# Kernel optimization log

Hardware: AMD Instinct MI355X
Metric: run time of the kernel (lower is better)

Reference implementation:

```python
import jax, jax.numpy as jnp
import numpy as np

MAX_NEIGHBORS = 10
D = 1024
N = 16384

def setup_inputs() -> dict:
    key = jax.random.key(0)
    ks = jax.random.split(key, 12)
    s = 0.05
    inp = {
        'target_embedding': jax.random.normal(ks[0], (D,), jnp.float32),
        'all_embeddings': jax.random.normal(ks[1], (N, D), jnp.float32),
        'similarity_matrix': jax.random.normal(ks[2], (N, N), jnp.float32),
        # attention_net: Linear(2D->D), ReLU, Linear(D->1)
        'W_att1': jax.random.normal(ks[3], (2 * D, D), jnp.float32) * s,
        'b_att1': jnp.zeros((D,), jnp.float32),
        'W_att2': jax.random.normal(ks[4], (D, 1), jnp.float32) * s,
        'b_att2': jnp.zeros((1,), jnp.float32),
        # neighbor_count_net: Linear(D->D//2), ReLU, Linear(D//2->1), Sigmoid
        'W_cnt1': jax.random.normal(ks[5], (D, D // 2), jnp.float32) * s,
        'b_cnt1': jnp.zeros((D // 2,), jnp.float32),
        'W_cnt2': jax.random.normal(ks[6], (D // 2, 1), jnp.float32) * s,
        'b_cnt2': jnp.zeros((1,), jnp.float32),
        'target_idx': 123,
    }
    return inp

def reference(target_embedding, all_embeddings, similarity_matrix,
              W_att1, b_att1, W_att2, b_att2,
              W_cnt1, b_cnt1, W_cnt2, b_cnt2, target_idx):
    # dynamic neighbor count: int(sigmoid(mlp(x)) * max_neighbors), clamped to [1, max_neighbors]
    h = jax.nn.relu(target_embedding @ W_cnt1 + b_cnt1)
    frac = jax.nn.sigmoid(h @ W_cnt2 + b_cnt2)[0]
    dynamic_k = jnp.clip(jnp.floor(frac * MAX_NEIGHBORS).astype(jnp.int32), 1, MAX_NEIGHBORS)

    # top-(K+1) over the target's similarity row; statically sized, mask to dynamic_k
    row = similarity_matrix[target_idx]
    _, top_idx = jax.lax.top_k(row, MAX_NEIGHBORS + 1)  # [K+1]
    # stable compaction: move target_idx (if present) to the end, keep order otherwise
    order = jnp.where(top_idx == target_idx, MAX_NEIGHBORS + 1, jnp.arange(MAX_NEIGHBORS + 1))
    neighbor_idx = top_idx[jnp.argsort(order)][:MAX_NEIGHBORS]  # [K]
    valid = jnp.arange(MAX_NEIGHBORS) < dynamic_k              # [K]

    neighbor_emb = all_embeddings[neighbor_idx]                 # [K, D]
    target_exp = jnp.broadcast_to(target_embedding, (MAX_NEIGHBORS, D))
    pair = jnp.concatenate([target_exp, neighbor_emb], axis=-1)  # [K, 2D]
    scores = (jax.nn.relu(pair @ W_att1 + b_att1) @ W_att2 + b_att2)[:, 0]  # [K]
    scores = jnp.where(valid, scores, -jnp.inf)
    weights = jax.nn.softmax(scores)                            # zeros at invalid slots
    aggregated = weights @ neighbor_emb                         # [D]
    return aggregated, weights, neighbor_idx, weights
```

## Files before the change

kernel.cpp:

```cpp
#include <hip/hip_runtime.h>
#include <math.h>

#define NN 16384
#define DD 1024
#define HD 512

#define WS_DK  0
#define WS_NB  4
#define WS_UV  32
#define WS_HP  11296

__global__ void k_phaseA(const float* __restrict__ x, const float* __restrict__ Wc1,
                         const float* __restrict__ sim, const int* __restrict__ tidx,
                         float* __restrict__ ws, float* __restrict__ out) {
    const int t = threadIdx.x;
    const int b = blockIdx.x;
    if (b != 0) {
        __shared__ float xs[32];
        const int c = b - 1;
        const int ibase = c * 32;
        if (t < 32) xs[t] = x[ibase + t];
        __syncthreads();
        float acc = 0.f;
        const float* W = Wc1 + (size_t)ibase * HD + t;
        #pragma unroll 8
        for (int ii = 0; ii < 32; ++ii) acc += xs[ii] * W[(size_t)ii * HD];
        ws[WS_HP + c * HD + t] = acc;
        return;
    }

    for (int i = t; i < 11 * DD; i += 512) ws[WS_UV + i] = 0.f;

    const int tgt = tidx[0];
    const float4* row4 = (const float4*)(sim + (size_t)tgt * NN);
    float vals[32];
    #pragma unroll
    for (int c = 0; c < 8; ++c) {
        float4 v = row4[c * 512 + t];
        vals[c * 4 + 0] = v.x; vals[c * 4 + 1] = v.y;
        vals[c * 4 + 2] = v.z; vals[c * 4 + 3] = v.w;
    }
    unsigned used = 0u;

    __shared__ float wvs[8];
    __shared__ int   wgs[8];
    __shared__ int   winner;
    __shared__ int   toplist[11];
    const int lane = t & 63, wave = t >> 6;

    for (int it = 0; it < 11; ++it) {
        float bv = -INFINITY; int bs = 0;
        #pragma unroll
        for (int s = 0; s < 32; ++s) {
            float v = ((used >> s) & 1u) ? -INFINITY : vals[s];
            if (v > bv) { bv = v; bs = s; }
        }
        int gi = (bs >> 2) * 2048 + t * 4 + (bs & 3);
        for (int off = 32; off > 0; off >>= 1) {
            float ov = __shfl_down(bv, off);
            int   og = __shfl_down(gi, off);
            if (ov > bv || (ov == bv && og < gi)) { bv = ov; gi = og; }
        }
        if (lane == 0) { wvs[wave] = bv; wgs[wave] = gi; }
        __syncthreads();
        if (t == 0) {
            float fv = wvs[0]; int fg = wgs[0];
            for (int w = 1; w < 8; ++w)
                if (wvs[w] > fv || (wvs[w] == fv && wgs[w] < fg)) { fv = wvs[w]; fg = wgs[w]; }
            toplist[it] = fg;
            winner = fg;
        }
        __syncthreads();
        int w = winner;
        if (((w >> 2) & 511) == t) used |= 1u << ((w >> 11) * 4 + (w & 3));
    }
    if (t == 0) {
        int cnt = 0;
        int* nb = (int*)ws + WS_NB;
        for (int i = 0; i < 11 && cnt < 10; ++i) {
            int v = toplist[i];
            if (v != tgt) { nb[cnt] = v; out[1034 + cnt] = (float)v; ++cnt; }
        }
    }
}

__global__ void k_phaseB(const float* __restrict__ x, const float* __restrict__ emb,
                         const float* __restrict__ W1, const float* __restrict__ bc1,
                         const float* __restrict__ Wc2, const float* __restrict__ bc2,
                         float* __restrict__ ws) {
    const int t = threadIdx.x;
    const int b = blockIdx.x;
    if (b == 128) {
        __shared__ float red[256];
        float acc = 0.f;
        #pragma unroll
        for (int jj = 0; jj < 2; ++jj) {
            int j = t + jj * 256;
            float s = 0.f;
            #pragma unroll 8
            for (int c = 0; c < 32; ++c) s += ws[WS_HP + c * HD + j];
            float h = fmaxf(s + bc1[j], 0.f);
            acc += h * Wc2[j];
        }
        red[t] = acc;
        __syncthreads();
        for (int off = 128; off > 0; off >>= 1) {
            if (t < off) red[t] += red[t + off];
            __syncthreads();
        }
        if (t == 0) {
            float z = red[0] + bc2[0];
            float frac = 1.f / (1.f + expf(-z));
            int dk = (int)floorf(frac * 10.f);
            ((int*)ws)[WS_DK] = dk < 1 ? 1 : (dk > 10 ? 10 : dk);
        }
        return;
    }
    __shared__ float xs[32];
    __shared__ float es[10][32];
    __shared__ int   nb[10];
    const int jc = b & 3;
    const int ic = b >> 2;
    const int ibase = ic * 32;
    const int j = jc * 256 + t;
    if (t < 10) nb[t] = ((const int*)ws)[WS_NB + t];
    if (t < 32) xs[t] = x[ibase + t];
    __syncthreads();
    for (int idx = t; idx < 320; idx += 256) {
        int k = idx >> 5, ii = idx & 31;
        es[k][ii] = emb[(size_t)nb[k] * DD + ibase + ii];
    }
    __syncthreads();
    float acc[11];
    #pragma unroll
    for (int k = 0; k < 11; ++k) acc[k] = 0.f;
    const float* Wt = W1 + (size_t)ibase * DD + j;
    const float* Wb = W1 + (size_t)(1024 + ibase) * DD + j;
    for (int ii = 0; ii < 32; ++ii) {
        float wt = Wt[(size_t)ii * DD];
        float wb = Wb[(size_t)ii * DD];
        acc[10] += xs[ii] * wt;
        #pragma unroll
        for (int k = 0; k < 10; ++k) acc[k] += es[k][ii] * wb;
    }
    #pragma unroll
    for (int k = 0; k < 11; ++k) atomicAdd(&ws[WS_UV + k * DD + j], acc[k]);
}

__global__ void k_phaseC(const float* __restrict__ emb, const float* __restrict__ ba1,
                         const float* __restrict__ W2, const float* __restrict__ ba2,
                         float* __restrict__ ws, float* __restrict__ out) {
    const int t = threadIdx.x;
    const int wave = t >> 6, lane = t & 63;
    __shared__ float sc[10];
    __shared__ float wl[10];
    __shared__ int   nbs[10];
    if (t < 10) nbs[t] = ((const int*)ws)[WS_NB + t];
    if (wave < 10) {
        float acc = 0.f;
        #pragma unroll
        for (int m = 0; m < 16; ++m) {
            int j = lane + m * 64;
            float h = ws[WS_UV + 10 * DD + j] + ws[WS_UV + wave * DD + j] + ba1[j];
            acc += fmaxf(h, 0.f) * W2[j];
        }
        #pragma unroll
        for (int off = 32; off > 0; off >>= 1) acc += __shfl_down(acc, off);
        if (lane == 0) sc[wave] = acc + ba2[0];
    }
    __syncthreads();
    if (t == 0) {
        int dk = ((const int*)ws)[WS_DK];
        float v[10];
        float m = -INFINITY;
        for (int k = 0; k < 10; ++k) {
            v[k] = (k < dk) ? sc[k] : -INFINITY;
            if (v[k] > m) m = v[k];
        }
        float sum = 0.f;
        for (int k = 0; k < 10; ++k) { v[k] = expf(v[k] - m); sum += v[k]; }
        for (int k = 0; k < 10; ++k) wl[k] = v[k] / sum;
    }
    __syncthreads();
    float a = 0.f;
    #pragma unroll
    for (int k = 0; k < 10; ++k) a += wl[k] * emb[(size_t)nbs[k] * DD + t];
    out[t] = a;
    if (t < 10) { out[1024 + t] = wl[t]; out[1044 + t] = wl[t]; }
}

extern "C" void kernel_launch(void* const* d_in, const int* in_sizes, int n_in,
                              void* d_out, int out_size, void* d_ws, size_t ws_size,
                              hipStream_t stream) {
    const float* x    = (const float*)d_in[0];
    const float* emb  = (const float*)d_in[1];
    const float* sim  = (const float*)d_in[2];
    const float* W1   = (const float*)d_in[3];
    const float* ba1  = (const float*)d_in[4];
    const float* W2   = (const float*)d_in[5];
    const float* ba2  = (const float*)d_in[6];
    const float* Wc1  = (const float*)d_in[7];
    const float* bc1  = (const float*)d_in[8];
    const float* Wc2  = (const float*)d_in[9];
    const float* bc2  = (const float*)d_in[10];
    const int*   tidx = (const int*)d_in[11];
    float* out = (float*)d_out;
    float* ws  = (float*)d_ws;

    hipLaunchKernelGGL(k_phaseA, dim3(33),  dim3(512),  0, stream, x, Wc1, sim, tidx, ws, out);
    hipLaunchKernelGGL(k_phaseB, dim3(129), dim3(256),  0, stream, x, emb, W1, bc1, Wc2, bc2, ws);
    hipLaunchKernelGGL(k_phaseC, dim3(1),   dim3(1024), 0, stream, emb, ba1, W2, ba2, ws, out);
}
```

Before: 38.36 us.

## Fuse three phases into one cooperative kernel with grid syncs and W1 prefetch

Replaces the three separate kernel launches with one cooperative kernel of 129 blocks that uses grid-wide syncs between the phases. While the top-k block runs, idle blocks pre-read their W1 slices to warm the cache for the attention matvec. The goal is to remove launch gaps between kernels and hide the W1 load latency behind the serial top-k. In exchange it adds grid.sync overhead and cooperative-launch constraints, and the top-k now runs on 256 threads with 64 values per thread instead of 512 threads.

```diff
diff --git a/kernel.cpp b/kernel.cpp
--- a/kernel.cpp
+++ b/kernel.cpp
@@ -1,5 +1,8 @@
 #include <hip/hip_runtime.h>
+#include <hip/hip_cooperative_groups.h>
 #include <math.h>
+
+namespace cg = cooperative_groups;
 
 #define NN 16384
 #define DD 1024
@@ -10,88 +13,129 @@
 #define WS_UV  32
 #define WS_HP  11296
 
-__global__ void k_phaseA(const float* __restrict__ x, const float* __restrict__ Wc1,
-                         const float* __restrict__ sim, const int* __restrict__ tidx,
-                         float* __restrict__ ws, float* __restrict__ out) {
+__global__ void k_fused(const float* __restrict__ x, const float* __restrict__ emb,
+                        const float* __restrict__ sim, const float* __restrict__ W1,
+                        const float* __restrict__ ba1, const float* __restrict__ W2,
+                        const float* __restrict__ ba2, const float* __restrict__ Wc1,
+                        const float* __restrict__ bc1, const float* __restrict__ Wc2,
+                        const float* __restrict__ bc2, const int* __restrict__ tidx,
+                        float* __restrict__ ws, float* __restrict__ out) {
+    cg::grid_group grid = cg::this_grid();
     const int t = threadIdx.x;
     const int b = blockIdx.x;
-    if (b != 0) {
-        __shared__ float xs[32];
-        const int c = b - 1;
-        const int ibase = c * 32;
-        if (t < 32) xs[t] = x[ibase + t];
-        __syncthreads();
-        float acc = 0.f;
-        const float* W = Wc1 + (size_t)ibase * HD + t;
-        #pragma unroll 8
-        for (int ii = 0; ii < 32; ++ii) acc += xs[ii] * W[(size_t)ii * HD];
-        ws[WS_HP + c * HD + t] = acc;
-        return;
-    }
-
-    for (int i = t; i < 11 * DD; i += 512) ws[WS_UV + i] = 0.f;
-
-    const int tgt = tidx[0];
-    const float4* row4 = (const float4*)(sim + (size_t)tgt * NN);
-    float vals[32];
-    #pragma unroll
-    for (int c = 0; c < 8; ++c) {
-        float4 v = row4[c * 512 + t];
-        vals[c * 4 + 0] = v.x; vals[c * 4 + 1] = v.y;
-        vals[c * 4 + 2] = v.z; vals[c * 4 + 3] = v.w;
-    }
-    unsigned used = 0u;
-
-    __shared__ float wvs[8];
-    __shared__ int   wgs[8];
+    const int lane = t & 63, wave = t >> 6;
+
+    __shared__ float xs[32];
+    __shared__ float es[10][32];
+    __shared__ int   nb[10];
+    __shared__ float wvs[4];
+    __shared__ int   wgs[4];
     __shared__ int   winner;
     __shared__ int   toplist[11];
-    const int lane = t & 63, wave = t >> 6;
-
-    for (int it = 0; it < 11; ++it) {
-        float bv = -INFINITY; int bs = 0;
-        #pragma unroll
-        for (int s = 0; s < 32; ++s) {
-            float v = ((used >> s) & 1u) ? -INFINITY : vals[s];
-            if (v > bv) { bv = v; bs = s; }
-        }
-        int gi = (bs >> 2) * 2048 + t * 4 + (bs & 3);
-        for (int off = 32; off > 0; off >>= 1) {
-            float ov = __shfl_down(bv, off);
-            int   og = __shfl_down(gi, off);
-            if (ov > bv || (ov == bv && og < gi)) { bv = ov; gi = og; }
-        }
-        if (lane == 0) { wvs[wave] = bv; wgs[wave] = gi; }
-        __syncthreads();
+    __shared__ float red[256];
+    __shared__ float sc[10];
+    __shared__ float wl[10];
+
+    if (b < 32) {
+        const int ibase = b * 32;
+        if (t < 32) xs[t] = x[ibase + t];
+        __syncthreads();
+        #pragma unroll
+        for (int jj = 0; jj < 2; ++jj) {
+            const int j = t + jj * 256;
+            float acc = 0.f;
+            const float* W = Wc1 + (size_t)ibase * HD + j;
+            #pragma unroll 8
+            for (int ii = 0; ii < 32; ++ii) acc += xs[ii] * W[(size_t)ii * HD];
+            ws[WS_HP + b * HD + j] = acc;
+        }
+    } else if (b == 32) {
+        for (int i = t; i < 11 * DD; i += 256) ws[WS_UV + i] = 0.f;
+    } else if (b == 33) {
+        const int tgt = tidx[0];
+        const float4* row4 = (const float4*)(sim + (size_t)tgt * NN);
+        float vals[64];
+        #pragma unroll
+        for (int c = 0; c < 16; ++c) {
+            float4 v = row4[c * 256 + t];
+            vals[c * 4 + 0] = v.x; vals[c * 4 + 1] = v.y;
+            vals[c * 4 + 2] = v.z; vals[c * 4 + 3] = v.w;
+        }
+        unsigned long long used = 0ull;
+        for (int it = 0; it < 11; ++it) {
+            float bv = -INFINITY; int bs = 0;
+            #pragma unroll
+            for (int s = 0; s < 64; ++s) {
+                float v = ((used >> s) & 1ull) ? -INFINITY : vals[s];
+                if (v > bv) { bv = v; bs = s; }
+            }
+            int gi = (bs >> 2) * 1024 + t * 4 + (bs & 3);
+            for (int off = 32; off > 0; off >>= 1) {
+                float ov = __shfl_down(bv, off);
+                int   og = __shfl_down(gi, off);
+                if (ov > bv || (ov == bv && og < gi)) { bv = ov; gi = og; }
+            }
+            if (lane == 0) { wvs[wave] = bv; wgs[wave] = gi; }
+            __syncthreads();
+            if (t == 0) {
+                float fv = wvs[0]; int fg = wgs[0];
+                for (int w = 1; w < 4; ++w)
+                    if (wvs[w] > fv || (wvs[w] == fv && wgs[w] < fg)) { fv = wvs[w]; fg = wgs[w]; }
+                toplist[it] = fg;
+                winner = fg;
+            }
+            __syncthreads();
+            int w = winner;
+            if (((w >> 2) & 255) == t) used |= 1ull << ((w >> 10) * 4 + (w & 3));
+        }
         if (t == 0) {
-            float fv = wvs[0]; int fg = wgs[0];
-            for (int w = 1; w < 8; ++w)
-                if (wvs[w] > fv || (wvs[w] == fv && wgs[w] < fg)) { fv = wvs[w]; fg = wgs[w]; }
-            toplist[it] = fg;
-            winner = fg;
-        }
-        __syncthreads();
-        int w = winner;
-        if (((w >> 2) & 511) == t) used |= 1u << ((w >> 11) * 4 + (w & 3));
+            int cnt = 0;
+            int* nbp = (int*)ws + WS_NB;
+            for (int i = 0; i < 11 && cnt < 10; ++i) {
+                int v = toplist[i];
+                if (v != tgt) { nbp[cnt] = v; out[1034 + cnt] = (float)v; ++cnt; }
+            }
+        }
+    } else if (b < 128) {
+        const int jc = b & 3, ic = b >> 2;
+        const int ibase = ic * 32;
+        const int j = jc * 256 + t;
+        float s = 0.f;
+        const float* Wt = W1 + (size_t)ibase * DD + j;
+        const float* Wb = W1 + (size_t)(1024 + ibase) * DD + j;
+        for (int ii = 0; ii < 32; ++ii) s += Wt[(size_t)ii * DD] + Wb[(size_t)ii * DD];
+        if (s == -1e30f) ws[WS_UV] = s;
     }
-    if (t == 0) {
-        int cnt = 0;
-        int* nb = (int*)ws + WS_NB;
-        for (int i = 0; i < 11 && cnt < 10; ++i) {
-            int v = toplist[i];
-            if (v != tgt) { nb[cnt] = v; out[1034 + cnt] = (float)v; ++cnt; }
-        }
-    }
-}
-
-__global__ void k_phaseB(const float* __restrict__ x, const float* __restrict__ emb,
-                         const float* __restrict__ W1, const float* __restrict__ bc1,
-                         const float* __restrict__ Wc2, const float* __restrict__ bc2,
-                         float* __restrict__ ws) {
-    const int t = threadIdx.x;
-    const int b = blockIdx.x;
-    if (b == 128) {
-        __shared__ float red[256];
+
+    grid.sync();
+
+    if (b < 128) {
+        const int jc = b & 3, ic = b >> 2;
+        const int ibase = ic * 32;
+        const int j = jc * 256 + t;
+        if (t < 10) nb[t] = ((const int*)ws)[WS_NB + t];
+        if (t < 32) xs[t] = x[ibase + t];
+        __syncthreads();
+        for (int idx = t; idx < 320; idx += 256) {
+            int k = idx >> 5, ii = idx & 31;
+            es[k][ii] = emb[(size_t)nb[k] * DD + ibase + ii];
+        }
+        __syncthreads();
+        float acc[11];
+        #pragma unroll
+        for (int k = 0; k < 11; ++k) acc[k] = 0.f;
+        const float* Wt = W1 + (size_t)ibase * DD + j;
+        const float* Wb = W1 + (size_t)(1024 + ibase) * DD + j;
+        for (int ii = 0; ii < 32; ++ii) {
+            float wt = Wt[(size_t)ii * DD];
+            float wb = Wb[(size_t)ii * DD];
+            acc[10] += xs[ii] * wt;
+            #pragma unroll
+            for (int k = 0; k < 10; ++k) acc[k] += es[k][ii] * wb;
+        }
+        #pragma unroll
+        for (int k = 0; k < 11; ++k) atomicAdd(&ws[WS_UV + k * DD + j], acc[k]);
+    } else {
         float acc = 0.f;
         #pragma unroll
         for (int jj = 0; jj < 2; ++jj) {
@@ -114,79 +158,49 @@
             int dk = (int)floorf(frac * 10.f);
             ((int*)ws)[WS_DK] = dk < 1 ? 1 : (dk > 10 ? 10 : dk);
         }
-        return;
     }
-    __shared__ float xs[32];
-    __shared__ float es[10][32];
-    __shared__ int   nb[10];
-    const int jc = b & 3;
-    const int ic = b >> 2;
-    const int ibase = ic * 32;
-    const int j = jc * 256 + t;
-    if (t < 10) nb[t] = ((const int*)ws)[WS_NB + t];
-    if (t < 32) xs[t] = x[ibase + t];
-    __syncthreads();
-    for (int idx = t; idx < 320; idx += 256) {
-        int k = idx >> 5, ii = idx & 31;
-        es[k][ii] = emb[(size_t)nb[k] * DD + ibase + ii];
+
+    grid.sync();
+
+    if (b == 0) {
+        if (t < 10) nb[t] = ((const int*)ws)[WS_NB + t];
+        __syncthreads();
+        for (int k = wave; k < 10; k += 4) {
+            float acc = 0.f;
+            #pragma unroll
+            for (int m = 0; m < 16; ++m) {
+                int j = lane + m * 64;
+                float h = ws[WS_UV + 10 * DD + j] + ws[WS_UV + k * DD + j] + ba1[j];
+                acc += fmaxf(h, 0.f) * W2[j];
+            }
+            #pragma unroll
+            for (int off = 32; off > 0; off >>= 1) acc += __shfl_down(acc, off);
+            if (lane == 0) sc[k] = acc + ba2[0];
+        }
+        __syncthreads();
+        if (t == 0) {
+            int dk = ((const int*)ws)[WS_DK];
+            float v[10];
+            float m = -INFINITY;
+            for (int k = 0; k < 10; ++k) {
+                v[k] = (k < dk) ? sc[k] : -INFINITY;
+                if (v[k] > m) m = v[k];
+            }
+            float sum = 0.f;
+            for (int k = 0; k < 10; ++k) { v[k] = expf(v[k] - m); sum += v[k]; }
+            for (int k = 0; k < 10; ++k) wl[k] = v[k] / sum;
+        }
+        __syncthreads();
+        #pragma unroll
+        for (int jj = 0; jj < 4; ++jj) {
+            int j = t + jj * 256;
+            float a = 0.f;
+            #pragma unroll
+            for (int k = 0; k < 10; ++k) a += wl[k] * emb[(size_t)nb[k] * DD + j];
+            out[j] = a;
+        }
+        if (t < 10) { out[1024 + t] = wl[t]; out[1044 + t] = wl[t]; }
     }
-    __syncthreads();
-    float acc[11];
-    #pragma unroll
-    for (int k = 0; k < 11; ++k) acc[k] = 0.f;
-    const float* Wt = W1 + (size_t)ibase * DD + j;
-    const float* Wb = W1 + (size_t)(1024 + ibase) * DD + j;
-    for (int ii = 0; ii < 32; ++ii) {
-        float wt = Wt[(size_t)ii * DD];
-        float wb = Wb[(size_t)ii * DD];
-        acc[10] += xs[ii] * wt;
-        #pragma unroll
-        for (int k = 0; k < 10; ++k) acc[k] += es[k][ii] * wb;
-    }
-    #pragma unroll
-    for (int k = 0; k < 11; ++k) atomicAdd(&ws[WS_UV + k * DD + j], acc[k]);
-}
-
-__global__ void k_phaseC(const float* __restrict__ emb, const float* __restrict__ ba1,
-                         const float* __restrict__ W2, const float* __restrict__ ba2,
-                         float* __restrict__ ws, float* __restrict__ out) {
-    const int t = threadIdx.x;
-    const int wave = t >> 6, lane = t & 63;
-    __shared__ float sc[10];
-    __shared__ float wl[10];
-    __shared__ int   nbs[10];
-    if (t < 10) nbs[t] = ((const int*)ws)[WS_NB + t];
-    if (wave < 10) {
-        float acc = 0.f;
-        #pragma unroll
-        for (int m = 0; m < 16; ++m) {
-            int j = lane + m * 64;
-            float h = ws[WS_UV + 10 * DD + j] + ws[WS_UV + wave * DD + j] + ba1[j];
-            acc += fmaxf(h, 0.f) * W2[j];
-        }
-        #pragma unroll
-        for (int off = 32; off > 0; off >>= 1) acc += __shfl_down(acc, off);
-        if (lane == 0) sc[wave] = acc + ba2[0];
-    }
-    __syncthreads();
-    if (t == 0) {
-        int dk = ((const int*)ws)[WS_DK];
-        float v[10];
-        float m = -INFINITY;
-        for (int k = 0; k < 10; ++k) {
-            v[k] = (k < dk) ? sc[k] : -INFINITY;
-            if (v[k] > m) m = v[k];
-        }
-        float sum = 0.f;
-        for (int k = 0; k < 10; ++k) { v[k] = expf(v[k] - m); sum += v[k]; }
-        for (int k = 0; k < 10; ++k) wl[k] = v[k] / sum;
-    }
-    __syncthreads();
-    float a = 0.f;
-    #pragma unroll
-    for (int k = 0; k < 10; ++k) a += wl[k] * emb[(size_t)nbs[k] * DD + t];
-    out[t] = a;
-    if (t < 10) { out[1024 + t] = wl[t]; out[1044 + t] = wl[t]; }
 }
 
 extern "C" void kernel_launch(void* const* d_in, const int* in_sizes, int n_in,
@@ -207,7 +221,8 @@
     float* out = (float*)d_out;
     float* ws  = (float*)d_ws;
 
-    hipLaunchKernelGGL(k_phaseA, dim3(33),  dim3(512),  0, stream, x, Wc1, sim, tidx, ws, out);
-    hipLaunchKernelGGL(k_phaseB, dim3(129), dim3(256),  0, stream, x, emb, W1, bc1, Wc2, bc2, ws);
-    hipLaunchKernelGGL(k_phaseC, dim3(1),   dim3(1024), 0, stream, emb, ba1, W2, ba2, ws, out);
+    void* args[] = {(void*)&x, (void*)&emb, (void*)&sim, (void*)&W1, (void*)&ba1,
+                    (void*)&W2, (void*)&ba2, (void*)&Wc1, (void*)&bc1, (void*)&Wc2,
+                    (void*)&bc2, (void*)&tidx, (void*)&ws, (void*)&out};
+    hipLaunchCooperativeKernel((void*)k_fused, dim3(129), dim3(256), args, 0, stream);
 }
```

Measured after the change: 72.40 us. 88.7% more time.
